# Kernel tuning notes

Hardware: AMD Instinct MI355X
Metric: run time of the kernel (lower is better)

The kernel has to match this reference:

```python
import jax, jax.numpy as jnp
import numpy as np

B, S, H, L = 64, 512, 1024, 9


def setup_inputs() -> dict:
    key = jax.random.key(0)
    k1, k2, k3, k4 = jax.random.split(key, 4)
    sequence_output = jax.random.normal(k1, (B, S, H), dtype=jnp.float32)
    valid_mask = jax.random.randint(k2, (B, S), 0, 2, dtype=jnp.int32)
    # classifier params (Dense(num_labels), TruncatedNormal(stddev=0.02) ~ normal here)
    W = jax.random.normal(k3, (H, L), dtype=jnp.float32) * 0.02
    b = jnp.zeros((L,), dtype=jnp.float32)
    return {"sequence_output": sequence_output, "valid_mask": valid_mask, "W": W, "b": b}


def _compact_valid(sequence_output, valid_mask):
    # Stable-sort tokens so valid (mask==1) tokens come first in original order,
    # then zero-pad the tail -- vectorized equivalent of the per-token Python loop.
    Bq, Sq, _ = sequence_output.shape
    pos = jnp.arange(Sq, dtype=jnp.int32)[None, :]                 # [1,S]
    sort_key = (1 - valid_mask) * Sq + pos                         # invalid pushed back, stable
    order = jnp.argsort(sort_key, axis=1)                          # [B,S]
    gathered = jnp.take_along_axis(sequence_output, order[:, :, None], axis=1)
    n_valid = jnp.sum(valid_mask, axis=1, keepdims=True)           # [B,1]
    keep = (pos < n_valid)[:, :, None]                             # [B,S,1]
    return jnp.where(keep, gathered, jnp.zeros((), sequence_output.dtype))


def reference(sequence_output, valid_mask, W, b):
    valid_output = _compact_valid(sequence_output, valid_mask)     # [B,S,H]
    # dropout is identity at inference (training=False)
    logits = jnp.einsum("bsh,hl->bsl", valid_output, W) + b
    return jax.nn.softmax(logits, axis=-1)
```

## Files before the change

### kernel.cpp

```cpp
#include <hip/hip_runtime.h>
#include <hip/hip_bf16.h>

#define BB 64
#define SS 512
#define HH 1024
#define LL 9

template <int CTRL>
__device__ __forceinline__ float dpp_add(float v) {
    int s = __builtin_bit_cast(int, v);
    int r = __builtin_amdgcn_update_dpp(0, s, CTRL, 0xF, 0xF, true);
    return v + __builtin_bit_cast(float, r);
}

__global__ __launch_bounds__(512) void fused_ner_kernel(
    const float* __restrict__ x, const int* __restrict__ mask,
    const float* __restrict__ W, const float* __restrict__ bias,
    float* __restrict__ out) {
    __shared__ __align__(16) float Wl[HH * LL];
    __shared__ int gidx_sh[SS];
    __shared__ int wsum[8];
    __shared__ float bsh[LL];
    __shared__ float obuf[128 * LL];

    const int tid  = threadIdx.x;
    const int bat  = blockIdx.x & 63;
    const int segA = blockIdx.x >> 6;
    const int segB = 7 - segA;
    const int lane = tid & 63;
    const int wv_  = tid >> 6;

    for (int f4 = tid; f4 < HH * LL / 4; f4 += 512) {
        __builtin_amdgcn_global_load_lds(
            (const __attribute__((address_space(1))) void*)(W + f4 * 4),
            (__attribute__((address_space(3))) void*)(&Wl[f4 * 4]),
            16, 0, 0);
    }
    if (tid < LL) bsh[tid] = bias[tid];

    const int m = mask[bat * SS + tid];
    int incl = m;
    #pragma unroll
    for (int off = 1; off < 64; off <<= 1) {
        int u = __shfl_up(incl, off, 64);
        if (lane >= off) incl += u;
    }
    if (lane == 63) wsum[wv_] = incl;
    __syncthreads();
    int nv = 0, wbase = 0;
    #pragma unroll
    for (int i = 0; i < 8; ++i) { if (i < wv_) wbase += wsum[i]; nv += wsum[i]; }
    const int excl = incl - m + wbase;
    if (m) gidx_sh[excl] = tid;
    __syncthreads();

    const int g = lane >> 4;
    const int k = lane & 15;
    const int segbase = (wv_ < 4 ? segA : segB) * 64;
    const int pw = segbase + (wv_ & 3) * 16;
    const int p0 = pw + g * 4;

    float acc[4][LL];
    #pragma unroll
    for (int r = 0; r < 4; ++r)
        #pragma unroll
        for (int l = 0; l < LL; ++l) acc[r][l] = 0.f;

    float sc[4];
    const float4* xr[4];
    #pragma unroll
    for (int r = 0; r < 4; ++r) {
        const int p = p0 + r;
        const bool valid = (p < nv);
        sc[r] = valid ? 1.f : 0.f;
        const int src = valid ? gidx_sh[p] : 0;
        xr[r] = reinterpret_cast<const float4*>(x + ((size_t)bat * SS + src) * HH);
    }

    if (pw < nv) {
        float4 xv[4][4];
        #pragma unroll
        for (int c = 0; c < 3; ++c)
            #pragma unroll
            for (int r = 0; r < 4; ++r) xv[c][r] = xr[r][c * 16 + k];

        #pragma unroll 4
        for (int c = 0; c < 16; ++c) {
            const int nc = (c + 3) & 15;
            #pragma unroll
            for (int r = 0; r < 4; ++r) xv[nc & 3][r] = xr[r][nc * 16 + k];

            float4 wb[9];
            const float* wp = &Wl[(c * 16 + k) * 36];
            #pragma unroll
            for (int j = 0; j < 9; ++j)
                wb[j] = *reinterpret_cast<const float4*>(wp + j * 4);
            const float* wf = reinterpret_cast<const float*>(wb);

            #pragma unroll
            for (int l = 0; l < LL; ++l) {
                #pragma unroll
                for (int r = 0; r < 4; ++r) {
                    const float4 xvv = xv[c & 3][r];
                    acc[r][l] += xvv.x * wf[0 * 9 + l] + xvv.y * wf[1 * 9 + l]
                               + xvv.z * wf[2 * 9 + l] + xvv.w * wf[3 * 9 + l];
                }
            }
        }
        #pragma unroll
        for (int r = 0; r < 4; ++r)
            #pragma unroll
            for (int l = 0; l < LL; ++l) {
                float v = acc[r][l];
                v = dpp_add<0x111>(v);
                v = dpp_add<0x112>(v);
                v = dpp_add<0x114>(v);
                v = dpp_add<0x118>(v);
                acc[r][l] = v;
            }
    }

    if (k == 15) {
        #pragma unroll
        for (int r = 0; r < 4; ++r) {
            float lg[LL];
            float mx = -3.0e38f;
            #pragma unroll
            for (int l = 0; l < LL; ++l) {
                lg[l] = acc[r][l] * sc[r] + bsh[l];
                mx = fmaxf(mx, lg[l]);
            }
            float ssum = 0.f;
            #pragma unroll
            for (int l = 0; l < LL; ++l) { lg[l] = __expf(lg[l] - mx); ssum += lg[l]; }
            const float inv = 1.f / ssum;
            const int lp = wv_ * 16 + g * 4 + r;
            #pragma unroll
            for (int l = 0; l < LL; ++l) obuf[lp * LL + l] = lg[l] * inv;
        }
    }
    __syncthreads();

    const size_t baseA = ((size_t)bat * SS + segA * 64) * LL;
    const size_t baseB = ((size_t)bat * SS + segB * 64) * LL;
    for (int t = tid; t < 64 * LL; t += 512) {
        out[baseA + t] = obuf[t];
        out[baseB + t] = obuf[64 * LL + t];
    }
}

extern "C" void kernel_launch(void* const* d_in, const int* in_sizes, int n_in,
                              void* d_out, int out_size, void* d_ws, size_t ws_size,
                              hipStream_t stream) {
    const float* x    = (const float*)d_in[0];
    const int*   mask = (const int*)d_in[1];
    const float* W    = (const float*)d_in[2];
    const float* bias = (const float*)d_in[3];
    float* out = (float*)d_out;

    fused_ner_kernel<<<256, 512, 0, stream>>>(x, mask, W, bias, out);
}
```

Measured before the change: 24.73 us.

## Compact valid rows across both segments to balance work across waves

```diff
diff --git a/kernel.cpp b/kernel.cpp
--- a/kernel.cpp
+++ b/kernel.cpp
@@ -56,59 +56,68 @@
 
     const int g = lane >> 4;
     const int k = lane & 15;
-    const int segbase = (wv_ < 4 ? segA : segB) * 64;
-    const int pw = segbase + (wv_ & 3) * 16;
-    const int p0 = pw + g * 4;
+    const int G = wv_ * 4 + g;
+    const int vA = min(max(nv - segA * 64, 0), 64);
+    const int vB = min(max(nv - segB * 64, 0), 64);
+    const int nwork = vA + vB;
 
-    float acc[4][LL];
-    #pragma unroll
-    for (int r = 0; r < 4; ++r)
+    #pragma unroll 1
+    for (int pass = 0; pass < 2; ++pass) {
+        const int jbase = pass * 64;
+        if (jbase + wv_ * 8 >= nwork) break;
+
+        float acc[2][LL];
         #pragma unroll
-        for (int l = 0; l < LL; ++l) acc[r][l] = 0.f;
+        for (int r = 0; r < 2; ++r)
+            #pragma unroll
+            for (int l = 0; l < LL; ++l) acc[r][l] = 0.f;
 
-    float sc[4];
-    const float4* xr[4];
-    #pragma unroll
-    for (int r = 0; r < 4; ++r) {
-        const int p = p0 + r;
-        const bool valid = (p < nv);
-        sc[r] = valid ? 1.f : 0.f;
-        const int src = valid ? gidx_sh[p] : 0;
-        xr[r] = reinterpret_cast<const float4*>(x + ((size_t)bat * SS + src) * HH);
-    }
+        float sc[2];
+        const float4* xr[2];
+        int jj[2];
+        #pragma unroll
+        for (int r = 0; r < 2; ++r) {
+            const int j = jbase + 2 * G + r;
+            jj[r] = j;
+            const bool valid = (j < nwork);
+            sc[r] = valid ? 1.f : 0.f;
+            const int p = (j < vA) ? segA * 64 + j : segB * 64 + (j - vA);
+            const int src = gidx_sh[valid ? p : 0];
+            xr[r] = reinterpret_cast<const float4*>(x + ((size_t)bat * SS + src) * HH);
+        }
 
-    if (pw < nv) {
-        float4 xv[4][4];
+        float4 xv[8][2];
         #pragma unroll
-        for (int c = 0; c < 3; ++c)
+        for (int c = 0; c < 8; ++c)
             #pragma unroll
-            for (int r = 0; r < 4; ++r) xv[c][r] = xr[r][c * 16 + k];
+            for (int r = 0; r < 2; ++r) xv[c][r] = xr[r][c * 16 + k];
 
-        #pragma unroll 4
+        #pragma unroll
         for (int c = 0; c < 16; ++c) {
-            const int nc = (c + 3) & 15;
-            #pragma unroll
-            for (int r = 0; r < 4; ++r) xv[nc & 3][r] = xr[r][nc * 16 + k];
-
+            const float4 xv0 = xv[c & 7][0];
+            const float4 xv1 = xv[c & 7][1];
+            if (c < 8) {
+                #pragma unroll
+                for (int r = 0; r < 2; ++r) xv[c & 7][r] = xr[r][(c + 8) * 16 + k];
+            }
             float4 wb[9];
             const float* wp = &Wl[(c * 16 + k) * 36];
             #pragma unroll
-            for (int j = 0; j < 9; ++j)
-                wb[j] = *reinterpret_cast<const float4*>(wp + j * 4);
+            for (int j2 = 0; j2 < 9; ++j2)
+                wb[j2] = *reinterpret_cast<const float4*>(wp + j2 * 4);
             const float* wf = reinterpret_cast<const float*>(wb);
 
             #pragma unroll
             for (int l = 0; l < LL; ++l) {
-                #pragma unroll
-                for (int r = 0; r < 4; ++r) {
-                    const float4 xvv = xv[c & 3][r];
-                    acc[r][l] += xvv.x * wf[0 * 9 + l] + xvv.y * wf[1 * 9 + l]
-                               + xvv.z * wf[2 * 9 + l] + xvv.w * wf[3 * 9 + l];
-                }
+                acc[0][l] += xv0.x * wf[0 * 9 + l] + xv0.y * wf[1 * 9 + l]
+                           + xv0.z * wf[2 * 9 + l] + xv0.w * wf[3 * 9 + l];
+                acc[1][l] += xv1.x * wf[0 * 9 + l] + xv1.y * wf[1 * 9 + l]
+                           + xv1.z * wf[2 * 9 + l] + xv1.w * wf[3 * 9 + l];
             }
         }
+
         #pragma unroll
-        for (int r = 0; r < 4; ++r)
+        for (int r = 0; r < 2; ++r)
             #pragma unroll
             for (int l = 0; l < LL; ++l) {
                 float v = acc[r][l];
@@ -118,34 +127,45 @@
                 v = dpp_add<0x118>(v);
                 acc[r][l] = v;
             }
+
+        if (k == 15) {
+            #pragma unroll
+            for (int r = 0; r < 2; ++r) {
+                float lg[LL];
+                float mx = -3.0e38f;
+                #pragma unroll
+                for (int l = 0; l < LL; ++l) {
+                    lg[l] = acc[r][l] * sc[r] + bsh[l];
+                    mx = fmaxf(mx, lg[l]);
+                }
+                float ssum = 0.f;
+                #pragma unroll
+                for (int l = 0; l < LL; ++l) { lg[l] = __expf(lg[l] - mx); ssum += lg[l]; }
+                const float inv = 1.f / ssum;
+                #pragma unroll
+                for (int l = 0; l < LL; ++l) obuf[jj[r] * LL + l] = lg[l] * inv;
+            }
+        }
     }
 
-    if (k == 15) {
-        #pragma unroll
-        for (int r = 0; r < 4; ++r) {
-            float lg[LL];
-            float mx = -3.0e38f;
-            #pragma unroll
-            for (int l = 0; l < LL; ++l) {
-                lg[l] = acc[r][l] * sc[r] + bsh[l];
-                mx = fmaxf(mx, lg[l]);
-            }
-            float ssum = 0.f;
-            #pragma unroll
-            for (int l = 0; l < LL; ++l) { lg[l] = __expf(lg[l] - mx); ssum += lg[l]; }
-            const float inv = 1.f / ssum;
-            const int lp = wv_ * 16 + g * 4 + r;
-            #pragma unroll
-            for (int l = 0; l < LL; ++l) obuf[lp * LL + l] = lg[l] * inv;
-        }
-    }
+    float bs[LL];
+    float mxb = -3.0e38f;
+    #pragma unroll
+    for (int l = 0; l < LL; ++l) { bs[l] = bsh[l]; mxb = fmaxf(mxb, bs[l]); }
+    float sb = 0.f;
+    #pragma unroll
+    for (int l = 0; l < LL; ++l) { bs[l] = __expf(bs[l] - mxb); sb += bs[l]; }
+    const float invb = 1.f / sb;
+
     __syncthreads();
 
     const size_t baseA = ((size_t)bat * SS + segA * 64) * LL;
     const size_t baseB = ((size_t)bat * SS + segB * 64) * LL;
     for (int t = tid; t < 64 * LL; t += 512) {
-        out[baseA + t] = obuf[t];
-        out[baseB + t] = obuf[64 * LL + t];
+        const int row = t / LL;
+        const int l   = t - row * LL;
+        out[baseA + t] = (row < vA) ? obuf[t] : bs[l] * invb;
+        out[baseB + t] = (row < vB) ? obuf[vA * LL + t] : bs[l] * invb;
     }
 }
 
```

New measurement: 24.37 us. Within noise of the previous version (-1.5%).
